# Optimization experiments

Hardware: AMD Instinct MI355X
Metric: run time of the kernel (lower is better)

The kernel has to match this reference:

```python
import jax, jax.numpy as jnp
import numpy as np

B, N, E, D = 4, 2048, 2048, 2048  # batch, seq, embedding_dim, out_dim


def setup_inputs() -> dict:
    key = jax.random.key(0)
    k1, k2, k3 = jax.random.split(key, 3)
    x = jax.random.normal(k1, (B, N, E), dtype=jnp.float32)
    # qkv_proj: Linear(E, 3*D). Store weight as [E, 3D] for x @ W.
    W = jax.random.normal(k2, (E, 3 * D), dtype=jnp.float32) * (1.0 / np.sqrt(E))
    b = jax.random.normal(k3, (3 * D,), dtype=jnp.float32) * 0.01
    return {"x": x, "W": W, "b": b}


def reference(x, W, b):
    d = W.shape[1] // 3
    n = x.shape[1]
    qkv = x @ W + b                                   # [B, N, 3D]
    q, k, v = jnp.split(qkv, 3, axis=-1)              # each [B, N, D]
    scale = 1.0 / np.sqrt(d).astype(np.float32)
    att = jnp.einsum('bqd,bkd->bqk', q, k) * scale    # [B, N, N]
    causal = jnp.tril(jnp.ones((n, n), dtype=bool))
    att = jnp.where(causal[None, :, :], att, -jnp.inf)
    # softmax_with_denom: stable softmax, also return the denominator
    m = jnp.max(att, axis=-1, keepdims=True)
    e = jnp.exp(att - m)
    denom = jnp.sum(e, axis=-1)                       # [B, N]
    p = e / denom[..., None]
    y = jnp.einsum('bqk,bkd->bqd', p, v)              # [B, N, D]
    return y, denom
```

## Files before the change

kernel.cpp:

```cpp
#include <hip/hip_runtime.h>

typedef unsigned short u16;
typedef unsigned int   u32;

#define SEQ 2048
#define EMB 2048
#define TD  6144

using bf16x8 = __attribute__((ext_vector_type(8))) __bf16;
using f32x4  = __attribute__((ext_vector_type(4))) float;

typedef __attribute__((address_space(1))) const void* gas_t;
typedef __attribute__((address_space(3))) void*       las_t;
#define GLOAD16(g, l) __builtin_amdgcn_global_load_lds((gas_t)(g), (las_t)(l), 16, 0, 0)

__device__ __forceinline__ u16 f2bf(float f) {
  u32 u = __float_as_uint(f);
  u += 0x7fffu + ((u >> 16) & 1u);
  return (u16)(u >> 16);
}

__global__ __launch_bounds__(256) void cast_x_kern(const float* __restrict__ x,
                                                   u16* __restrict__ xb) {
  size_t i = ((size_t)blockIdx.x * 256 + threadIdx.x) * 4;
  float4 v = *(const float4*)(x + i);
  ushort4 u;
  u.x = f2bf(v.x); u.y = f2bf(v.y); u.z = f2bf(v.z); u.w = f2bf(v.w);
  *(ushort4*)(xb + i) = u;
}

__global__ __launch_bounds__(256) void castT_W_kern(const float* __restrict__ W,
                                                    u16* __restrict__ Wt) {
  __shared__ float t[64][65];
  int c0 = blockIdx.x * 64, r0 = blockIdx.y * 64;
  int tid = threadIdx.x;
#pragma unroll
  for (int i = 0; i < 4; ++i) {
    int flat = i * 1024 + tid * 4;
    int r = flat >> 6, c = flat & 63;
    float4 v = *(const float4*)(W + (size_t)(r0 + r) * TD + c0 + c);
    t[r][c] = v.x; t[r][c + 1] = v.y; t[r][c + 2] = v.z; t[r][c + 3] = v.w;
  }
  __syncthreads();
#pragma unroll
  for (int i = 0; i < 4; ++i) {
    int flat = i * 1024 + tid * 4;
    int wr = flat >> 6, wc = flat & 63;
    ushort4 u;
    u.x = f2bf(t[wc + 0][wr]); u.y = f2bf(t[wc + 1][wr]);
    u.z = f2bf(t[wc + 2][wr]); u.w = f2bf(t[wc + 3][wr]);
    *(ushort4*)(Wt + (size_t)(c0 + wr) * EMB + r0 + wc) = u;
  }
}

__global__ __launch_bounds__(256) void transpose_v_kern(const u16* __restrict__ qkv,
                                                        u16* __restrict__ vT) {
  __shared__ u16 t[64][68];
  int b = blockIdx.z;
  int d0 = blockIdx.x * 64, n0 = blockIdx.y * 64;
  const u16* src = qkv + (size_t)b * SEQ * TD + 2 * SEQ;
  u16* dst = vT + (size_t)b * SEQ * SEQ;
  int tid = threadIdx.x;
#pragma unroll
  for (int i = 0; i < 4; ++i) {
    int flat = i * 1024 + tid * 4;
    int n = flat >> 6, d = flat & 63;
    *(ushort4*)&t[n][d] = *(const ushort4*)(src + (size_t)(n0 + n) * TD + d0 + d);
  }
  __syncthreads();
#pragma unroll
  for (int i = 0; i < 4; ++i) {
    int flat = i * 1024 + tid * 4;
    int d = flat >> 6, n = flat & 63;
    ushort4 u;
    u.x = t[n + 0][d]; u.y = t[n + 1][d]; u.z = t[n + 2][d]; u.w = t[n + 3][d];
    *(ushort4*)(dst + (size_t)(d0 + d) * SEQ + n0 + n) = u;
  }
}

template <int MODE>
__global__ __launch_bounds__(512, 2) void gemm256(const u16* __restrict__ Ab,
                                                  const u16* __restrict__ Bb,
                                                  void* __restrict__ Cb,
                                                  const float* __restrict__ bias) {
  __shared__ char lds[2][65536];

  constexpr int lda = (MODE == 0) ? EMB : (MODE == 1) ? TD : 4096;
  constexpr int ldb = (MODE == 0) ? EMB : (MODE == 1) ? TD : SEQ;
  constexpr int NWG = (MODE == 0) ? 768 : (MODE == 1) ? 144 : 256;
  constexpr int CPX = NWG / 8;

  int bid = blockIdx.x;
  int wg = (bid & 7) * CPX + (bid >> 3);

  const u16 *A, *Bt;
  int row0, col0, nk;
  size_t coff = 0;
  if constexpr (MODE == 0) {
    A = Ab; Bt = Bb;
    row0 = (wg / 24) * 256; col0 = (wg % 24) * 256; nk = EMB / 64;
  } else if constexpr (MODE == 1) {
    int b = wg / 36, tq = wg % 36;
    int qi = (int)((sqrtf(8.f * (float)tq + 1.f) - 1.f) * 0.5f);
    while ((qi + 1) * (qi + 2) / 2 <= tq) ++qi;
    while (qi * (qi + 1) / 2 > tq) --qi;
    int kj = tq - qi * (qi + 1) / 2;
    A = Ab + (size_t)b * SEQ * TD;
    Bt = A + EMB;
    row0 = qi * 256; col0 = kj * 256; nk = EMB / 64;
    coff = (size_t)b * SEQ * SEQ;
  } else {
    int b = wg >> 6, qi = (wg >> 3) & 7, nj = wg & 7;
    A = Ab + (size_t)b * SEQ * 4096;
    Bt = Bb + (size_t)b * SEQ * SEQ;
    row0 = qi * 256; col0 = nj * 256; nk = (qi + 1) * 4;
    coff = (size_t)b * SEQ * SEQ;
  }

  int tid = threadIdx.x;
  int wave = tid >> 6, lane = tid & 63;
  int wm = wave >> 2, wn = wave & 3;

  int sbase[8];
#pragma unroll
  for (int i = 0; i < 4; ++i) sbase[i] = 32768 + i * 8192 + wave * 1024;
#pragma unroll
  for (int i = 0; i < 4; ++i)
    sbase[4 + i] = i * 4096 + ((wave < 4) ? wave * 1024 : 16384 + (wave - 4) * 1024);

  auto stageb = [&](int bi, int t, int buf) {
    int ob = sbase[bi];
    int obl = ob + lane * 16;
    int row = (obl & 32767) >> 7;
    int cb = obl & 127;
    int c = ((cb ^ ((row & 7) << 4)) >> 1) + t * 64;
    const u16* src = (ob < 32768) ? (A + (size_t)(row0 + row) * lda + c)
                                  : (Bt + (size_t)(col0 + row) * ldb + c);
    GLOAD16(src, (char*)&lds[buf][0] + ob);
  };

  auto ldA = [&](int buf, int rr, int ks) -> bf16x8 {
    int cb = ks * 64 + (lane >> 4) * 16;
    return *(const bf16x8*)&lds[buf][rr * 128 + (cb ^ ((rr & 7) << 4))];
  };
  auto ldB = [&](int buf, int rr, int ks) -> bf16x8 {
    int cb = ks * 64 + (lane >> 4) * 16;
    return *(const bf16x8*)&lds[buf][32768 + rr * 128 + (cb ^ ((rr & 7) << 4))];
  };

  f32x4 acc[8][4];
#pragma unroll
  for (int m = 0; m < 8; ++m)
#pragma unroll
    for (int n = 0; n < 4; ++n) acc[m][n] = (f32x4){0.f, 0.f, 0.f, 0.f};

#pragma unroll
  for (int bi = 0; bi < 8; ++bi) stageb(bi, 0, 0);
#pragma unroll
  for (int bi = 0; bi < 6; ++bi) stageb(bi, 1, 1);
  asm volatile("s_waitcnt vmcnt(6)" ::: "memory");
  __builtin_amdgcn_s_barrier();

  bf16x8 bfg[4][2];
  for (int t = 0; t < nk; ++t) {
    int cur = t & 1, nxt = cur ^ 1;
#pragma unroll
    for (int p = 0; p < 4; ++p) {
      bf16x8 afg[2][2];
      if (p == 0) {
#pragma unroll
        for (int n = 0; n < 4; ++n)
#pragma unroll
          for (int ks = 0; ks < 2; ++ks)
            bfg[n][ks] = ldB(cur, wn * 64 + n * 16 + (lane & 15), ks);
      }
#pragma unroll
      for (int m = 0; m < 2; ++m)
#pragma unroll
        for (int ks = 0; ks < 2; ++ks)
          afg[m][ks] = ldA(cur, wm * 128 + (p * 2 + m) * 16 + (lane & 15), ks);
      if (p == 0) {
        if (t + 1 < nk) { stageb(6, t + 1, nxt); stageb(7, t + 1, nxt); }
        asm volatile("s_waitcnt lgkmcnt(8)" ::: "memory");
      } else if (t + 2 < nk) {
        stageb(2 * (p - 1), t + 2, cur);
        stageb(2 * (p - 1) + 1, t + 2, cur);
      }
      __builtin_amdgcn_s_barrier();
      asm volatile("s_waitcnt lgkmcnt(0)" ::: "memory");
      __builtin_amdgcn_s_setprio(1);
#pragma unroll
      for (int m = 0; m < 2; ++m)
#pragma unroll
        for (int n = 0; n < 4; ++n)
#pragma unroll
          for (int ks = 0; ks < 2; ++ks)
            acc[p * 2 + m][n] = __builtin_amdgcn_mfma_f32_16x16x32_bf16(
                afg[m][ks], bfg[n][ks], acc[p * 2 + m][n], 0, 0, 0);
      __builtin_amdgcn_s_setprio(0);
      if (p == 3) {
        if (t + 2 < nk)       asm volatile("s_waitcnt vmcnt(6)" ::: "memory");
        else if (t + 1 < nk)  asm volatile("s_waitcnt vmcnt(0)" ::: "memory");
      }
      __builtin_amdgcn_s_barrier();
    }
  }

  int l4 = (lane >> 4) << 2, ln = lane & 15;
  int rb = row0 + wm * 128, cb0 = col0 + wn * 64;
  if constexpr (MODE == 0) {
    u16* C = (u16*)Cb;
#pragma unroll
    for (int n = 0; n < 4; ++n) {
      float bv = bias[cb0 + n * 16 + ln];
#pragma unroll
      for (int m = 0; m < 8; ++m)
#pragma unroll
        for (int r = 0; r < 4; ++r)
          C[(size_t)(rb + m * 16 + l4 + r) * TD + cb0 + n * 16 + ln] =
              f2bf(acc[m][n][r] + bv);
    }
  } else if constexpr (MODE == 1) {
    float* C = (float*)Cb + coff;
    const float scale = 0.022097086912079608f;
#pragma unroll
    for (int m = 0; m < 8; ++m)
#pragma unroll
      for (int n = 0; n < 4; ++n)
#pragma unroll
        for (int r = 0; r < 4; ++r)
          C[(size_t)(rb + m * 16 + l4 + r) * SEQ + cb0 + n * 16 + ln] =
              acc[m][n][r] * scale;
  } else {
    float* C = (float*)Cb + coff;
#pragma unroll
    for (int m = 0; m < 8; ++m)
#pragma unroll
      for (int n = 0; n < 4; ++n)
#pragma unroll
        for (int r = 0; r < 4; ++r)
          C[(size_t)(rb + m * 16 + l4 + r) * SEQ + cb0 + n * 16 + ln] = acc[m][n][r];
  }
}

__global__ __launch_bounds__(256) void softmax_kern(const float* __restrict__ att,
                                                    u16* __restrict__ P,
                                                    float* __restrict__ denom) {
  int row = blockIdx.x;
  int q = row & (SEQ - 1);
  const float* arow = att + (size_t)row * SEQ;
  u16* prow = P + (size_t)row * 4096;
  int jlen = ((q >> 8) + 1) << 8;
  int tid = threadIdx.x;
  int j0 = tid * 4, j1 = tid * 4 + 1024;
  float NI = -__builtin_inff();
  float4 a0 = make_float4(NI, NI, NI, NI), a1 = a0;
  if (j0 < jlen) a0 = *(const float4*)(arow + j0);
  if (j1 < jlen) a1 = *(const float4*)(arow + j1);
  if (j0 + 0 > q) a0.x = NI;
  if (j0 + 1 > q) a0.y = NI;
  if (j0 + 2 > q) a0.z = NI;
  if (j0 + 3 > q) a0.w = NI;
  if (j1 + 0 > q) a1.x = NI;
  if (j1 + 1 > q) a1.y = NI;
  if (j1 + 2 > q) a1.z = NI;
  if (j1 + 3 > q) a1.w = NI;
  float mx = fmaxf(fmaxf(fmaxf(a0.x, a0.y), fmaxf(a0.z, a0.w)),
                   fmaxf(fmaxf(a1.x, a1.y), fmaxf(a1.z, a1.w)));
#pragma unroll
  for (int off = 32; off; off >>= 1) mx = fmaxf(mx, __shfl_xor(mx, off, 64));
  __shared__ float red[8];
  int wv = tid >> 6;
  if ((tid & 63) == 0) red[wv] = mx;
  __syncthreads();
  mx = fmaxf(fmaxf(red[0], red[1]), fmaxf(red[2], red[3]));
  a0.x = expf(a0.x - mx); a0.y = expf(a0.y - mx);
  a0.z = expf(a0.z - mx); a0.w = expf(a0.w - mx);
  a1.x = expf(a1.x - mx); a1.y = expf(a1.y - mx);
  a1.z = expf(a1.z - mx); a1.w = expf(a1.w - mx);
  float s = (a0.x + a0.y + a0.z + a0.w) + (a1.x + a1.y + a1.z + a1.w);
#pragma unroll
  for (int off = 32; off; off >>= 1) s += __shfl_xor(s, off, 64);
  if ((tid & 63) == 0) red[4 + wv] = s;
  __syncthreads();
  s = red[4] + red[5] + red[6] + red[7];
  float inv = 1.0f / s;
  if (j0 < jlen) {
    ushort4 u;
    u.x = f2bf(a0.x * inv); u.y = f2bf(a0.y * inv);
    u.z = f2bf(a0.z * inv); u.w = f2bf(a0.w * inv);
    *(ushort4*)(prow + j0) = u;
  }
  if (j1 < jlen) {
    ushort4 u;
    u.x = f2bf(a1.x * inv); u.y = f2bf(a1.y * inv);
    u.z = f2bf(a1.z * inv); u.w = f2bf(a1.w * inv);
    *(ushort4*)(prow + j1) = u;
  }
  if (tid == 0) denom[row] = s;
}

extern "C" void kernel_launch(void* const* d_in, const int* in_sizes, int n_in,
                              void* d_out, int out_size, void* d_ws, size_t ws_size,
                              hipStream_t stream) {
  const float* x    = (const float*)d_in[0];
  const float* W    = (const float*)d_in[1];
  const float* bias = (const float*)d_in[2];

  if (ws_size < 201326592u) return;

  char* w = (char*)d_ws;
  u16*   qkv = (u16*)w;
  u16*   xb  = (u16*)(w + 100663296);
  u16*   Wt  = (u16*)(w + 134217728);
  u16*   vT  = (u16*)(w + 100663296);
  float* att = (float*)(w + 134217728);
  u16*   P   = (u16*)(w + 134217728);

  float* y     = (float*)d_out;
  float* denom = y + (size_t)4 * SEQ * SEQ;

  cast_x_kern<<<16384, 256, 0, stream>>>(x, xb);
  castT_W_kern<<<dim3(96, 32), 256, 0, stream>>>(W, Wt);
  gemm256<0><<<768, 512, 0, stream>>>(xb, Wt, qkv, bias);
  transpose_v_kern<<<dim3(32, 32, 4), 256, 0, stream>>>(qkv, vT);
  gemm256<1><<<144, 512, 0, stream>>>(qkv, nullptr, att, nullptr);
  softmax_kern<<<8192, 256, 0, stream>>>(att, P, denom);
  gemm256<2><<<256, 512, 0, stream>>>(P, vT, y, nullptr);
}
```

Measured before the change: 358.3 us.

## Restructure GEMM LDS double-buffering into separate A/B arrays with ping-pong tile steps

Replaces the single 2x64KB LDS byte array and the prefetch-two-tiles-ahead schedule with four named shared arrays (A/B per buffer) and a ping-pong tile_step lambda that prefetches only the next tile. Distinct static LDS arrays let the compiler resolve addresses statically, and the prefetch is split across the first two sub-phases. A full vmcnt(0) wait and barrier now close every tile, which shortens prefetch depth and may expose global-load latency.

Result: slower. 365.8 us (+2.1%).

```diff
diff --git a/kernel.cpp b/kernel.cpp
--- a/kernel.cpp
+++ b/kernel.cpp
@@ -83,7 +83,10 @@
                                                   const u16* __restrict__ Bb,
                                                   void* __restrict__ Cb,
                                                   const float* __restrict__ bias) {
-  __shared__ char lds[2][65536];
+  __shared__ u16 sA0[16384];
+  __shared__ u16 sB0[16384];
+  __shared__ u16 sA1[16384];
+  __shared__ u16 sB1[16384];
 
   constexpr int lda = (MODE == 0) ? EMB : (MODE == 1) ? TD : 4096;
   constexpr int ldb = (MODE == 0) ? EMB : (MODE == 1) ? TD : SEQ;
@@ -120,33 +123,27 @@
   int tid = threadIdx.x;
   int wave = tid >> 6, lane = tid & 63;
   int wm = wave >> 2, wn = wave & 3;
-
-  int sbase[8];
-#pragma unroll
-  for (int i = 0; i < 4; ++i) sbase[i] = 32768 + i * 8192 + wave * 1024;
-#pragma unroll
-  for (int i = 0; i < 4; ++i)
-    sbase[4 + i] = i * 4096 + ((wave < 4) ? wave * 1024 : 16384 + (wave - 4) * 1024);
-
-  auto stageb = [&](int bi, int t, int buf) {
-    int ob = sbase[bi];
+  int ln = lane & 15;
+
+  auto stageB = [&](auto& SB, int i, int t) {
+    int ob = i * 8192 + wave * 1024;
     int obl = ob + lane * 16;
-    int row = (obl & 32767) >> 7;
-    int cb = obl & 127;
+    int row = obl >> 7, cb = obl & 127;
     int c = ((cb ^ ((row & 7) << 4)) >> 1) + t * 64;
-    const u16* src = (ob < 32768) ? (A + (size_t)(row0 + row) * lda + c)
-                                  : (Bt + (size_t)(col0 + row) * ldb + c);
-    GLOAD16(src, (char*)&lds[buf][0] + ob);
+    GLOAD16(Bt + (size_t)(col0 + row) * ldb + c, (char*)SB + ob);
   };
-
-  auto ldA = [&](int buf, int rr, int ks) -> bf16x8 {
+  auto stageA = [&](auto& SA, int i, int t) {
+    int ob = i * 4096 + ((wave < 4) ? wave * 1024 : 16384 + (wave - 4) * 1024);
+    int obl = ob + lane * 16;
+    int row = obl >> 7, cb = obl & 127;
+    int c = ((cb ^ ((row & 7) << 4)) >> 1) + t * 64;
+    GLOAD16(A + (size_t)(row0 + row) * lda + c, (char*)SA + ob);
+  };
+
+  auto ldfrag = [&](auto& S, int rr, int ks) -> bf16x8 {
     int cb = ks * 64 + (lane >> 4) * 16;
-    return *(const bf16x8*)&lds[buf][rr * 128 + (cb ^ ((rr & 7) << 4))];
+    return *(const bf16x8*)((const char*)S + rr * 128 + (cb ^ ((rr & 7) << 4)));
   };
-  auto ldB = [&](int buf, int rr, int ks) -> bf16x8 {
-    int cb = ks * 64 + (lane >> 4) * 16;
-    return *(const bf16x8*)&lds[buf][32768 + rr * 128 + (cb ^ ((rr & 7) << 4))];
-  };
 
   f32x4 acc[8][4];
 #pragma unroll
@@ -154,38 +151,43 @@
 #pragma unroll
     for (int n = 0; n < 4; ++n) acc[m][n] = (f32x4){0.f, 0.f, 0.f, 0.f};
 
-#pragma unroll
-  for (int bi = 0; bi < 8; ++bi) stageb(bi, 0, 0);
-#pragma unroll
-  for (int bi = 0; bi < 6; ++bi) stageb(bi, 1, 1);
-  asm volatile("s_waitcnt vmcnt(6)" ::: "memory");
-  __builtin_amdgcn_s_barrier();
-
-  bf16x8 bfg[4][2];
-  for (int t = 0; t < nk; ++t) {
-    int cur = t & 1, nxt = cur ^ 1;
-#pragma unroll
-    for (int p = 0; p < 4; ++p) {
-      bf16x8 afg[2][2];
-      if (p == 0) {
-#pragma unroll
-        for (int n = 0; n < 4; ++n)
-#pragma unroll
-          for (int ks = 0; ks < 2; ++ks)
-            bfg[n][ks] = ldB(cur, wn * 64 + n * 16 + (lane & 15), ks);
-      }
+  auto tile_step = [&](auto& CA, auto& CB, auto& NA, auto& NB, int t) {
+    bool pf = (t + 1 < nk);
+    bf16x8 bfg[4][2], afg[2][2];
+#pragma unroll
+    for (int n = 0; n < 4; ++n)
+#pragma unroll
+      for (int ks = 0; ks < 2; ++ks)
+        bfg[n][ks] = ldfrag(CB, wn * 64 + n * 16 + ln, ks);
+#pragma unroll
+    for (int m = 0; m < 2; ++m)
+#pragma unroll
+      for (int ks = 0; ks < 2; ++ks)
+        afg[m][ks] = ldfrag(CA, wm * 128 + m * 16 + ln, ks);
+    if (pf) { stageB(NB, 0, t + 1); stageB(NB, 1, t + 1);
+              stageA(NA, 0, t + 1); stageA(NA, 1, t + 1); }
+    asm volatile("s_waitcnt lgkmcnt(8)" ::: "memory");
+    __builtin_amdgcn_s_barrier();
+    asm volatile("s_waitcnt lgkmcnt(0)" ::: "memory");
+    __builtin_amdgcn_s_setprio(1);
+#pragma unroll
+    for (int m = 0; m < 2; ++m)
+#pragma unroll
+      for (int n = 0; n < 4; ++n)
+#pragma unroll
+        for (int ks = 0; ks < 2; ++ks)
+          acc[m][n] = __builtin_amdgcn_mfma_f32_16x16x32_bf16(
+              afg[m][ks], bfg[n][ks], acc[m][n], 0, 0, 0);
+    __builtin_amdgcn_s_setprio(0);
+#pragma unroll
+    for (int p = 1; p < 4; ++p) {
 #pragma unroll
       for (int m = 0; m < 2; ++m)
 #pragma unroll
         for (int ks = 0; ks < 2; ++ks)
-          afg[m][ks] = ldA(cur, wm * 128 + (p * 2 + m) * 16 + (lane & 15), ks);
-      if (p == 0) {
-        if (t + 1 < nk) { stageb(6, t + 1, nxt); stageb(7, t + 1, nxt); }
-        asm volatile("s_waitcnt lgkmcnt(8)" ::: "memory");
-      } else if (t + 2 < nk) {
-        stageb(2 * (p - 1), t + 2, cur);
-        stageb(2 * (p - 1) + 1, t + 2, cur);
-      }
+          afg[m][ks] = ldfrag(CA, wm * 128 + p * 32 + m * 16 + ln, ks);
+      if (p == 1 && pf) { stageB(NB, 2, t + 1); stageB(NB, 3, t + 1);
+                          stageA(NA, 2, t + 1); stageA(NA, 3, t + 1); }
       __builtin_amdgcn_s_barrier();
       asm volatile("s_waitcnt lgkmcnt(0)" ::: "memory");
       __builtin_amdgcn_s_setprio(1);
@@ -199,14 +201,25 @@
                 afg[m][ks], bfg[n][ks], acc[p * 2 + m][n], 0, 0, 0);
       __builtin_amdgcn_s_setprio(0);
       if (p == 3) {
-        if (t + 2 < nk)       asm volatile("s_waitcnt vmcnt(6)" ::: "memory");
-        else if (t + 1 < nk)  asm volatile("s_waitcnt vmcnt(0)" ::: "memory");
+        asm volatile("s_waitcnt vmcnt(0)" ::: "memory");
+        __builtin_amdgcn_s_barrier();
       }
-      __builtin_amdgcn_s_barrier();
     }
-  }
-
-  int l4 = (lane >> 4) << 2, ln = lane & 15;
+  };
+
+#pragma unroll
+  for (int bi = 0; bi < 4; ++bi) stageB(sB0, bi, 0);
+#pragma unroll
+  for (int bi = 0; bi < 4; ++bi) stageA(sA0, bi, 0);
+  asm volatile("s_waitcnt vmcnt(0)" ::: "memory");
+  __builtin_amdgcn_s_barrier();
+
+  for (int t2 = 0; t2 < nk; t2 += 2) {
+    tile_step(sA0, sB0, sA1, sB1, t2);
+    tile_step(sA1, sB1, sA0, sB0, t2 + 1);
+  }
+
+  int l4 = (lane >> 4) << 2;
   int rb = row0 + wm * 128, cb0 = col0 + wn * 64;
   if constexpr (MODE == 0) {
     u16* C = (u16*)Cb;
```
